# Performance work log

Hardware: AMD Instinct MI355X
Metric: run time of the kernel (lower is better)

## Reference

```python
import jax, jax.numpy as jnp
import numpy as np

_DIR_INLIER = 0.9          # _HOUGHVOTING_DIRECTION_INLIER
_NUM_INLIER = 500          # _HOUGHVOTING_NUM_INLIER
_LABEL_THRESH = 500        # _LABEL2MASK_THRESHOL
NUM_CLASSES = 10
BS, H, W = 1, 240, 320


def setup_inputs() -> dict:
    key = jax.random.key(0)
    k_lab, k_cx, k_cy, k_nx, k_ny, k_nd = jax.random.split(key, 6)
    label = jax.random.randint(k_lab, (BS, H, W), 0, NUM_CLASSES + 1).astype(jnp.int32)
    xs = jnp.arange(W, dtype=jnp.float32)
    ys = jnp.arange(H, dtype=jnp.float32)
    xv, yv = jnp.meshgrid(xs, ys)  # [H, W] each
    # per-class ground-truth centers well inside the image so voting converges
    cxs = jax.random.uniform(k_cx, (NUM_CLASSES,), minval=40.0, maxval=W - 40.0)
    cys = jax.random.uniform(k_cy, (NUM_CLASSES,), minval=40.0, maxval=H - 40.0)
    dx = cxs[:, None, None] - xv[None]  # [C, H, W]
    dy = cys[:, None, None] - yv[None]
    nrm = jnp.sqrt(dx * dx + dy * dy) + 1e-6
    dirx = dx / nrm + 0.01 * jax.random.normal(k_nx, (NUM_CLASSES, H, W))
    diry = dy / nrm + 0.01 * jax.random.normal(k_ny, (NUM_CLASSES, H, W))
    depth = (1.0 + 0.3 * jnp.arange(NUM_CLASSES, dtype=jnp.float32))[:, None, None] \
        + 0.01 * jax.random.normal(k_nd, (NUM_CLASSES, H, W))
    cmap = jnp.stack([dirx, diry, depth], axis=1).reshape(3 * NUM_CLASSES, H, W)
    centermap = jnp.broadcast_to(cmap[None], (BS, 3 * NUM_CLASSES, H, W)).astype(jnp.float32)
    return {"label": label, "centermap": centermap}


def hough_voting(label, centermap, num_classes):
    bs, H_, W_ = label.shape
    xs = jnp.arange(W_, dtype=jnp.float32)
    ys = jnp.arange(H_, dtype=jnp.float32)
    xv, yv = jnp.meshgrid(xs, ys)            # [H, W]
    xsi = jnp.arange(W_, dtype=jnp.int32)
    all_centers, all_depths = [], []
    for b in range(bs):
        lab = label[b]
        row_c, row_d = [], []
        for cls in range(1, num_classes + 1):
            cmask = lab == cls                                    # [H, W]
            enough = cmask.sum() >= _LABEL_THRESH
            c3 = centermap[b, (cls - 1) * 3:(cls - 1) * 3 + 3]    # [3, H, W]
            slope = c3[1] / c3[0]                                  # dy/dx per pixel
            # every masked pixel votes along its line at every column x
            y_idx = jnp.round(yv[:, :, None] + slope[:, :, None] * (xs[None, None, :] - xv[:, :, None])).astype(jnp.int32)  # [H, W, W]
            valid = (y_idx >= 0) & (y_idx < H_) & cmask[:, :, None]
            bins = jnp.clip(y_idx, 0, H_ - 1) * W_ + xsi[None, None, :]
            hist = jnp.zeros(H_ * W_, jnp.float32).at[bins.ravel()].add(valid.ravel().astype(jnp.float32))
            cbin = jnp.argmax(hist)
            inlier_num = hist[cbin]
            cx = (cbin % W_).astype(jnp.float32)
            cy = (cbin // W_).astype(jnp.float32)
            # depth: mean of depth channel over direction-consistent class pixels
            disx = xv - cx
            disy = yv - cy
            dnrm = jnp.sqrt(disx * disx + disy * disy)
            dot = jnp.abs((disx / dnrm) * c3[0] + (disy / dnrm) * c3[1])  # nan at center -> compares False, as torch
            imask = (dot >= _DIR_INLIER) & cmask
            cnt = imask.sum().astype(jnp.float32)
            dsum = jnp.sum(jnp.where(imask, c3[2], 0.0))
            dmean = jnp.where(cnt > 0, dsum / jnp.maximum(cnt, 1.0), jnp.nan)
            trig = enough & (inlier_num > _NUM_INLIER)
            row_c.append(jnp.where(trig, jnp.stack([cx, cy]), jnp.zeros(2, jnp.float32)))
            row_d.append(jnp.where(trig, dmean, 0.0))
        all_centers.append(jnp.stack(row_c))
        all_depths.append(jnp.stack(row_d))
    return jnp.stack(all_centers), jnp.stack(all_depths)


def reference(label, centermap):
    return hough_voting(label, centermap, NUM_CLASSES)
```

## Files before the change

kernel.cpp:

```cpp
#include <hip/hip_runtime.h>
#include <stdint.h>

#define H 240
#define W 320
#define NPIX (H * W)
#define NCLS 10
#define COLS 4
#define BIN_BITS 20
#define BIN_MASK 0xFFFFFu


__global__ void k_init(uint32_t* ws) {
    int i = threadIdx.x;
    if (i < 128) ws[i] = 0;
}

__global__ __launch_bounds__(256) void k_compact(const int* __restrict__ label,
                                                 const float* __restrict__ cm,
                                                 uint32_t* __restrict__ cls_cnt,
                                                 uint2* __restrict__ list) {
    __shared__ uint32_t lcnt[NCLS];
    __shared__ uint32_t lbase[NCLS];
    int p = blockIdx.x * 256 + threadIdx.x;
    if (threadIdx.x < NCLS) lcnt[threadIdx.x] = 0;
    __syncthreads();

    int l = label[p];
    bool match = (l >= 1 && l <= NCLS);
    int cls = l - 1;
    uint32_t li = 0;
    if (match) li = atomicAdd(&lcnt[cls], 1u);
    __syncthreads();

    if (threadIdx.x < NCLS) {
        uint32_t c = lcnt[threadIdx.x];
        lbase[threadIdx.x] = c ? atomicAdd(&cls_cnt[threadIdx.x], c) : 0u;
    }
    __syncthreads();

    if (match) {
        float dirx = cm[(cls * 3 + 0) * NPIX + p];
        float diry = cm[(cls * 3 + 1) * NPIX + p];
        float slope = diry / dirx;
        int y = p / W, x = p - y * W;
        uint2 e;
        e.x = (uint32_t)(x | (y << 16));
        e.y = __float_as_uint(slope);
        list[cls * NPIX + lbase[cls] + li] = e;
    }
}

__global__ __launch_bounds__(256) void k_vote(const uint32_t* __restrict__ cls_cnt,
                                              const uint2* __restrict__ list,
                                              unsigned long long* __restrict__ best) {
    int cls = blockIdx.y;
    int x0 = blockIdx.x * COLS;
    __shared__ uint32_t hist[COLS][H];
    __shared__ unsigned long long red[256];
    for (int i = threadIdx.x; i < COLS * H; i += 256) ((uint32_t*)hist)[i] = 0;
    __syncthreads();

    int n = (int)cls_cnt[cls];
    const uint2* lst = list + cls * NPIX;
    for (int i = threadIdx.x; i < n; i += 256) {
        uint2 e = lst[i];
        float slope = __uint_as_float(e.y);
        float xf = (float)(e.x & 0xFFFFu);
        float yf = (float)(e.x >> 16);
#pragma unroll
        for (int c = 0; c < COLS; ++c) {
            float dx = (float)(x0 + c) - xf;
            float t = yf + slope * dx;
            float r = rintf(t);
            if (r >= 0.0f && r <= (float)(H - 1)) {
                atomicAdd(&hist[c][(int)r], 1u);
            }
        }
    }
    __syncthreads();

    unsigned long long k = 0;
    for (int i = threadIdx.x; i < COLS * H; i += 256) {
        int c = i / H, y = i - c * H;
        uint32_t v = hist[c][y];
        uint32_t bin = (uint32_t)(y * W + x0 + c);
        unsigned long long key =
            ((unsigned long long)v << BIN_BITS) | (unsigned long long)(BIN_MASK - bin);
        if (key > k) k = key;
    }
    red[threadIdx.x] = k;
    __syncthreads();
    for (int s = 128; s > 0; s >>= 1) {
        if (threadIdx.x < s) {
            if (red[threadIdx.x + s] > red[threadIdx.x]) red[threadIdx.x] = red[threadIdx.x + s];
        }
        __syncthreads();
    }
    if (threadIdx.x == 0) atomicMax(&best[cls], red[0]);
}

__global__ __launch_bounds__(256) void k_inlier(const int* __restrict__ label,
                                                const float* __restrict__ cm,
                                                const unsigned long long* __restrict__ best,
                                                uint32_t* __restrict__ icnt,
                                                float* __restrict__ dsum) {
    int cls = blockIdx.y;
    unsigned long long key = best[cls];
    uint32_t bin = BIN_MASK - (uint32_t)(key & BIN_MASK);
    float cx = (float)(bin % W);
    float cy = (float)(bin / W);

    const float* c0p = cm + (cls * 3 + 0) * NPIX;
    const float* c1p = cm + (cls * 3 + 1) * NPIX;
    const float* c2p = cm + (cls * 3 + 2) * NPIX;

    uint32_t lcnt = 0;
    float ldsum = 0.0f;
    int base = blockIdx.x * 2560;
    for (int i = 0; i < 10; ++i) {
        int p = base + i * 256 + threadIdx.x;
        if (label[p] == cls + 1) {
            int y = p / W, x = p - y * W;
            float disx = (float)x - cx;
            float disy = (float)y - cy;
            float dn = sqrtf(disx * disx + disy * disy);
            if (dn > 0.0f) {
                float dot = fabsf((disx / dn) * c0p[p] + (disy / dn) * c1p[p]);
                if (dot >= 0.9f) {
                    lcnt += 1;
                    ldsum += c2p[p];
                }
            }
        }
    }
    __shared__ float sd[256];
    __shared__ uint32_t sc[256];
    sd[threadIdx.x] = ldsum;
    sc[threadIdx.x] = lcnt;
    __syncthreads();
    for (int s = 128; s > 0; s >>= 1) {
        if (threadIdx.x < s) {
            sd[threadIdx.x] += sd[threadIdx.x + s];
            sc[threadIdx.x] += sc[threadIdx.x + s];
        }
        __syncthreads();
    }
    if (threadIdx.x == 0) {
        if (sc[0]) atomicAdd(&icnt[cls], sc[0]);
        if (sd[0] != 0.0f) atomicAdd(&dsum[cls], sd[0]);
    }
}

__global__ void k_final(const uint32_t* __restrict__ cls_cnt,
                        const unsigned long long* __restrict__ best,
                        const uint32_t* __restrict__ icnt,
                        const float* __restrict__ dsum,
                        float* __restrict__ out) {
    int cls = threadIdx.x;
    if (cls >= NCLS) return;
    unsigned long long key = best[cls];
    uint32_t hv = (uint32_t)(key >> BIN_BITS);
    uint32_t bin = BIN_MASK - (uint32_t)(key & BIN_MASK);
    float cx = (float)(bin % W);
    float cy = (float)(bin / W);
    bool trig = (cls_cnt[cls] >= 500u) && (hv > 500u);
    float c = (float)icnt[cls];
    float dm = (c > 0.0f) ? (dsum[cls] / fmaxf(c, 1.0f)) : __builtin_nanf("");
    out[cls * 2 + 0] = trig ? cx : 0.0f;
    out[cls * 2 + 1] = trig ? cy : 0.0f;
    out[2 * NCLS + cls] = trig ? dm : 0.0f;
}

extern "C" void kernel_launch(void* const* d_in, const int* in_sizes, int n_in,
                              void* d_out, int out_size, void* d_ws, size_t ws_size,
                              hipStream_t stream) {
    const int* label = (const int*)d_in[0];
    const float* cm = (const float*)d_in[1];
    float* out = (float*)d_out;
    char* ws = (char*)d_ws;

    uint32_t* cls_cnt = (uint32_t*)(ws + 0);
    unsigned long long* best = (unsigned long long*)(ws + 64);
    uint32_t* icnt = (uint32_t*)(ws + 192);
    float* dsum = (float*)(ws + 256);
    uint2* list = (uint2*)(ws + 512);

    k_init<<<1, 128, 0, stream>>>((uint32_t*)ws);
    k_compact<<<NPIX / 256, 256, 0, stream>>>(label, cm, cls_cnt, list);
    k_vote<<<dim3(W / COLS, NCLS), 256, 0, stream>>>(cls_cnt, list, best);
    k_inlier<<<dim3(30, NCLS), 256, 0, stream>>>(label, cm, best, icnt, dsum);
    k_final<<<1, 64, 0, stream>>>(cls_cnt, best, icnt, dsum, out);
}
```

Before: 108.0 us.

## Aggregate conflicting LDS histogram atomics per wavefront and use shuffle reductions

In the voting kernel, each wavefront now uses ballot and shuffle to find lanes voting into the same histogram bin. Up to three of the most common bins get one aggregated atomic each, and the remaining lanes fall back to per-lane atomics. This targets serialization of LDS atomics when many pixels vote into the same row bin near the center. The shared-memory tree reductions in the vote and inlier kernels are also replaced with wavefront shuffle reductions, which removes several barriers. The price is extra ballot and shuffle work on every column iteration, even when votes do not collide.

```diff
diff --git a/kernel.cpp b/kernel.cpp
--- a/kernel.cpp
+++ b/kernel.cpp
@@ -56,25 +56,40 @@
     int cls = blockIdx.y;
     int x0 = blockIdx.x * COLS;
     __shared__ uint32_t hist[COLS][H];
-    __shared__ unsigned long long red[256];
+    __shared__ unsigned long long wred[4];
     for (int i = threadIdx.x; i < COLS * H; i += 256) ((uint32_t*)hist)[i] = 0;
     __syncthreads();
 
     int n = (int)cls_cnt[cls];
     const uint2* lst = list + cls * NPIX;
-    for (int i = threadIdx.x; i < n; i += 256) {
-        uint2 e = lst[i];
+    for (int i0 = 0; i0 < n; i0 += 256) {
+        int i = i0 + (int)threadIdx.x;
+        bool inb = (i < n);
+        uint2 e;
+        e.x = 0u; e.y = 0u;
+        if (inb) e = lst[i];
         float slope = __uint_as_float(e.y);
         float xf = (float)(e.x & 0xFFFFu);
         float yf = (float)(e.x >> 16);
 #pragma unroll
         for (int c = 0; c < COLS; ++c) {
             float dx = (float)(x0 + c) - xf;
-            float t = yf + slope * dx;
-            float r = rintf(t);
-            if (r >= 0.0f && r <= (float)(H - 1)) {
-                atomicAdd(&hist[c][(int)r], 1u);
+            float r = rintf(yf + slope * dx);
+            bool valid = inb && (r >= 0.0f) && (r <= (float)(H - 1));
+            int bin = (int)r;
+            unsigned long long rem = __ballot(valid);
+#pragma unroll
+            for (int t3 = 0; t3 < 3; ++t3) {
+                if (rem == 0ull) break;
+                int src = __ffsll((unsigned long long)rem) - 1;
+                int b0 = __shfl(bin, src);
+                unsigned long long m = __ballot(valid && (bin == b0));
+                if ((int)(threadIdx.x & 63u) == src)
+                    atomicAdd(&hist[c][b0], (uint32_t)__popcll(m));
+                if (valid && (bin == b0)) valid = false;
+                rem &= ~m;
             }
+            if (valid) atomicAdd(&hist[c][bin], 1u);
         }
     }
     __syncthreads();
@@ -88,15 +103,19 @@
             ((unsigned long long)v << BIN_BITS) | (unsigned long long)(BIN_MASK - bin);
         if (key > k) k = key;
     }
-    red[threadIdx.x] = k;
-    __syncthreads();
-    for (int s = 128; s > 0; s >>= 1) {
-        if (threadIdx.x < s) {
-            if (red[threadIdx.x + s] > red[threadIdx.x]) red[threadIdx.x] = red[threadIdx.x + s];
-        }
-        __syncthreads();
-    }
-    if (threadIdx.x == 0) atomicMax(&best[cls], red[0]);
+#pragma unroll
+    for (int off = 32; off > 0; off >>= 1) {
+        unsigned long long o = __shfl_down(k, off);
+        if (o > k) k = o;
+    }
+    if ((threadIdx.x & 63u) == 0u) wred[threadIdx.x >> 6] = k;
+    __syncthreads();
+    if (threadIdx.x == 0) {
+        unsigned long long kk = wred[0];
+#pragma unroll
+        for (int w = 1; w < 4; ++w) if (wred[w] > kk) kk = wred[w];
+        atomicMax(&best[cls], kk);
+    }
 }
 
 __global__ __launch_bounds__(256) void k_inlier(const int* __restrict__ label,
@@ -133,21 +152,23 @@
             }
         }
     }
-    __shared__ float sd[256];
-    __shared__ uint32_t sc[256];
-    sd[threadIdx.x] = ldsum;
-    sc[threadIdx.x] = lcnt;
-    __syncthreads();
-    for (int s = 128; s > 0; s >>= 1) {
-        if (threadIdx.x < s) {
-            sd[threadIdx.x] += sd[threadIdx.x + s];
-            sc[threadIdx.x] += sc[threadIdx.x + s];
-        }
-        __syncthreads();
-    }
+#pragma unroll
+    for (int off = 32; off > 0; off >>= 1) {
+        ldsum += __shfl_down(ldsum, off);
+        lcnt += __shfl_down(lcnt, off);
+    }
+    __shared__ float sd[4];
+    __shared__ uint32_t sc[4];
+    if ((threadIdx.x & 63u) == 0u) {
+        sd[threadIdx.x >> 6] = ldsum;
+        sc[threadIdx.x >> 6] = lcnt;
+    }
+    __syncthreads();
     if (threadIdx.x == 0) {
-        if (sc[0]) atomicAdd(&icnt[cls], sc[0]);
-        if (sd[0] != 0.0f) atomicAdd(&dsum[cls], sd[0]);
+        float td = sd[0] + sd[1] + sd[2] + sd[3];
+        uint32_t tc = sc[0] + sc[1] + sc[2] + sc[3];
+        if (tc) atomicAdd(&icnt[cls], tc);
+        if (td != 0.0f) atomicAdd(&dsum[cls], td);
     }
 }
 
```

After: 135.5 us. +25.5%, slower.
